# Kernel tuning notes

Hardware: AMD Instinct MI355X
Metric: run time of the kernel (lower is better)

## Reference

```python
import jax, jax.numpy as jnp
import numpy as np

N_NODES = 100_000
N_EDGES = 1_600_000
F_NODE = 4
F_EDGE = 5
H = 64
EDGE_DIM = 2 * H + F_EDGE  # 133


def setup_inputs() -> dict:
    key = jax.random.key(0)
    ks = jax.random.split(key, 24)
    s = 0.05
    inp = {
        "node_feat": jax.random.normal(ks[0], (N_NODES, F_NODE), jnp.float32),
        "edge_feat": jax.random.normal(ks[1], (N_EDGES, F_EDGE), jnp.float32),
        "src": jax.random.randint(ks[2], (N_EDGES,), 0, N_NODES, jnp.int32),
        "dst": jax.random.randint(ks[3], (N_EDGES,), 0, N_NODES, jnp.int32),
        # SAGEConv 1 (DGL mean aggregator: fc_self(h) + fc_neigh(mean_neigh(h)) + bias)
        "W1s": jax.random.normal(ks[4], (F_NODE, H), jnp.float32) * s,
        "W1n": jax.random.normal(ks[5], (F_NODE, H), jnp.float32) * s,
        "b1": jnp.zeros((H,), jnp.float32),
        # SAGEConv 2
        "W2s": jax.random.normal(ks[6], (H, H), jnp.float32) * s,
        "W2n": jax.random.normal(ks[7], (H, H), jnp.float32) * s,
        "b2": jnp.zeros((H,), jnp.float32),
        # nodeprocess: Linear(F_NODE? no -> applied to h which is H-dim) Linear(H? )
        # NOTE: original declares nn.Linear(num_node_features, hidden) but applies it to h (H-dim);
        # we follow the applied shape, Linear(H, H), so the math is runnable and consistent.
        "Wnp": jax.random.normal(ks[8], (H, H), jnp.float32) * s,
        "bnp": jnp.zeros((H,), jnp.float32),
        # edgeprocess: Linear(EDGE_DIM, H) -> tanh -> Linear(H, 1)
        "We1": jax.random.normal(ks[9], (EDGE_DIM, H), jnp.float32) * s,
        "be1": jnp.zeros((H,), jnp.float32),
        "We2": jax.random.normal(ks[10], (H, 1), jnp.float32) * s,
        "be2": jnp.zeros((1,), jnp.float32),
        # lin1: Linear(EDGE_DIM, H); lin2: Linear(H, 1)
        "Wl1": jax.random.normal(ks[11], (EDGE_DIM, H), jnp.float32) * s,
        "bl1": jnp.zeros((H,), jnp.float32),
        "Wl2": jax.random.normal(ks[12], (H, 1), jnp.float32) * s,
        "bl2": jnp.zeros((1,), jnp.float32),
    }
    return inp


def _sage_mean(h, src, dst, Ws, Wn, b, inv_deg):
    # project first (cheaper: N x d instead of E x d), then gather+scatter-mean
    msg = (h @ Wn)[src]                                    # [E, H]
    agg = jax.ops.segment_sum(msg, dst, num_segments=h.shape[0]) * inv_deg
    return h @ Ws + agg + b


def reference(node_feat, edge_feat, src, dst,
              W1s, W1n, b1, W2s, W2n, b2,
              Wnp, bnp, We1, be1, We2, be2,
              Wl1, bl1, Wl2, bl2):
    n = node_feat.shape[0]
    deg = jax.ops.segment_sum(jnp.ones_like(dst, jnp.float32), dst, num_segments=n)
    inv_deg = (1.0 / jnp.maximum(deg, 1.0))[:, None]       # [N,1]

    h = jax.nn.relu(_sage_mean(node_feat, src, dst, W1s, W1n, b1, inv_deg))
    h = jax.nn.relu(_sage_mean(h, src, dst, W2s, W2n, b2, inv_deg))

    h_src = jax.nn.relu(h[src] @ Wnp + bnp)                # [E, H]
    h_dst = jax.nn.relu(h[dst] @ Wnp + bnp)                # [E, H]
    ef = jnp.concatenate([h_src, h_dst, edge_feat], axis=1)  # [E, 133]

    w = jax.nn.sigmoid(jnp.tanh(ef @ We1 + be1) @ We2 + be2)  # [E, 1]
    efw = ef * w
    out = jax.nn.relu(efw @ Wl1 + bl1)                     # dropout: eval mode (identity)
    return out @ Wl2 + bl2                                 # [E, 1]
```

## Files before the change

### kernel.cpp

```cpp
#include <hip/hip_runtime.h>
#include <math.h>


typedef __attribute__((ext_vector_type(8))) short bf16x8;
typedef __attribute__((ext_vector_type(4))) float f32x4;

__device__ __forceinline__ float fast_tanh(float x) {
    x = fminf(fmaxf(x, -15.f), 15.f);
    float e2 = __expf(2.f * x);
    return (e2 - 1.f) * __builtin_amdgcn_rcpf(e2 + 1.f);
}
__device__ __forceinline__ float fast_sigmoid(float x) {
    x = fminf(fmaxf(x, -60.f), 60.f);
    return __builtin_amdgcn_rcpf(1.f + __expf(-x));
}
__device__ __forceinline__ unsigned short f2bf(float f) {
    unsigned u = __float_as_uint(f);
    u = u + 0x7FFFu + ((u >> 16) & 1u);
    return (unsigned short)(u >> 16);
}
__device__ __forceinline__ unsigned pack2bf(float lo, float hi) {
    return ((unsigned)f2bf(hi) << 16) | (unsigned)f2bf(lo);
}
__device__ __forceinline__ float bflo(unsigned u) { return __uint_as_float(u << 16); }
__device__ __forceinline__ float bfhi(unsigned u) { return __uint_as_float(u & 0xFFFF0000u); }
__device__ __forceinline__ float bf2f(unsigned short h) {
    return __uint_as_float((unsigned)h << 16);
}

__device__ __forceinline__ f32x4 mfma16(uint4 a, uint4 b, f32x4 c) {
    return __builtin_amdgcn_mfma_f32_16x16x32_bf16(
        __builtin_bit_cast(bf16x8, a), __builtin_bit_cast(bf16x8, b), c, 0, 0, 0);
}

__device__ __forceinline__ float dpp_sum16(float x) {
    int t;
    t = __builtin_amdgcn_update_dpp(0, __float_as_int(x), 0xB1, 0xF, 0xF, true);
    x += __int_as_float(t);
    t = __builtin_amdgcn_update_dpp(0, __float_as_int(x), 0x4E, 0xF, 0xF, true);
    x += __int_as_float(t);
    t = __builtin_amdgcn_update_dpp(0, __float_as_int(x), 0x141, 0xF, 0xF, true);
    x += __int_as_float(t);
    t = __builtin_amdgcn_update_dpp(0, __float_as_int(x), 0x140, 0xF, 0xF, true);
    x += __int_as_float(t);
    return x;
}

__global__ void rank_k(const int* __restrict__ dst, int* __restrict__ deg,
                       int* __restrict__ rank, int E) {
    int e = blockIdx.x * blockDim.x + threadIdx.x;
    if (e < E) rank[e] = atomicAdd(&deg[dst[e]], 1);
}

__global__ void scan1_k(const int* __restrict__ deg, int* __restrict__ off,
                        int* __restrict__ bsum, int N) {
    __shared__ int tmp[256];
    int i = blockIdx.x * 256 + threadIdx.x;
    int v = (i < N) ? deg[i] : 0;
    tmp[threadIdx.x] = v;
    __syncthreads();
#pragma unroll
    for (int s = 1; s < 256; s <<= 1) {
        int t = (threadIdx.x >= s) ? tmp[threadIdx.x - s] : 0;
        __syncthreads();
        tmp[threadIdx.x] += t;
        __syncthreads();
    }
    if (i < N) off[i] = tmp[threadIdx.x] - v;
    if (threadIdx.x == 255) bsum[blockIdx.x] = tmp[255];
}

__global__ void scan2_k(int* __restrict__ bsum, int nb) {
    __shared__ int tmp[512];
    int i = threadIdx.x;
    int v = (i < nb) ? bsum[i] : 0;
    tmp[i] = v;
    __syncthreads();
#pragma unroll
    for (int s = 1; s < 512; s <<= 1) {
        int t = (i >= s) ? tmp[i - s] : 0;
        __syncthreads();
        tmp[i] += t;
        __syncthreads();
    }
    if (i < nb) bsum[i] = tmp[i] - v;
}

__global__ void scan3_k(int* __restrict__ off, const int* __restrict__ bsum,
                        int N, int E) {
    int i = blockIdx.x * 256 + threadIdx.x;
    if (i < N) off[i] += bsum[blockIdx.x];
    if (i == 0) off[N] = E;
}

__global__ void fill2_k(const int* __restrict__ src, const int* __restrict__ dst,
                        const int* __restrict__ off, const int* __restrict__ rank,
                        int4* __restrict__ slot4, int E) {
    int e = blockIdx.x * blockDim.x + threadIdx.x;
    if (e >= E) return;
    int d = dst[e];
    int pos = off[d] + rank[e];
    slot4[pos] = make_int4(src[e], e, d, 0);
}

__global__ void prep_w_k(const float* __restrict__ W2s, const float* __restrict__ W2n,
                         const float* __restrict__ Wnp, const float* __restrict__ We1,
                         const float* __restrict__ Wl1, uint4* __restrict__ w2sF,
                         uint4* __restrict__ w2nF, uint4* __restrict__ wnpF,
                         uint4* __restrict__ wbigF) {
    const int b = blockIdx.x, t = threadIdx.x;
    if (b < 3) {
        const float* W = (b == 0) ? W2s : (b == 1) ? W2n : Wnp;
        uint4* out = (b == 0) ? w2sF : (b == 1) ? w2nF : wnpF;
        for (int u = t; u < 2 * 4 * 64; u += 256) {
            int l = u & 63, nt = (u >> 6) & 3, ks = u >> 8;
            int m = nt * 16 + (l & 15), kb = ks * 32 + (l >> 4) * 8;
            unsigned hi[4], lo[4];
#pragma unroll
            for (int jp = 0; jp < 4; ++jp) {
                float v0 = W[(kb + 2 * jp) * 64 + m];
                float v1 = W[(kb + 2 * jp + 1) * 64 + m];
                unsigned short h0 = f2bf(v0), h1 = f2bf(v1);
                unsigned short q0 = f2bf(v0 - bf2f(h0)), q1 = f2bf(v1 - bf2f(h1));
                hi[jp] = ((unsigned)h1 << 16) | h0;
                lo[jp] = ((unsigned)q1 << 16) | q0;
            }
            out[u * 2]     = make_uint4(hi[0], hi[1], hi[2], hi[3]);
            out[u * 2 + 1] = make_uint4(lo[0], lo[1], lo[2], lo[3]);
        }
    } else {
        for (int u = t; u < 2 * 16 * 64; u += 256) {
            int l = u & 63, nt = (u >> 6) & 15, ks = u >> 10;
            int m = nt * 16 + (l & 15), kb = ks * 32 + (l >> 4) * 8;
            int half = m >> 7, cc = m & 127, jj = cc >> 1, p = cc & 1;
            const float* W = p ? Wl1 : We1;
            unsigned hi[4], lo[4];
#pragma unroll
            for (int jp = 0; jp < 4; ++jp) {
                float v0 = W[(half * 64 + kb + 2 * jp) * 64 + jj];
                float v1 = W[(half * 64 + kb + 2 * jp + 1) * 64 + jj];
                unsigned short h0 = f2bf(v0), h1 = f2bf(v1);
                unsigned short q0 = f2bf(v0 - bf2f(h0)), q1 = f2bf(v1 - bf2f(h1));
                hi[jp] = ((unsigned)h1 << 16) | h0;
                lo[jp] = ((unsigned)q1 << 16) | q0;
            }
            wbigF[u * 2]     = make_uint4(hi[0], hi[1], hi[2], hi[3]);
            wbigF[u * 2 + 1] = make_uint4(lo[0], lo[1], lo[2], lo[3]);
        }
    }
}

__global__ __launch_bounds__(256, 8)
void aggh1f_k(const int* __restrict__ off, const int4* __restrict__ slot4,
              const float* __restrict__ nf,
              const float* __restrict__ W1s, const float* __restrict__ W1n,
              const float* __restrict__ b1, unsigned* __restrict__ h1b, int N) {
    int n = blockIdx.x * 16 + (threadIdx.x >> 4);
    if (n >= N) return;
    int q = threadIdx.x & 15;
    int s0 = off[n], s1 = off[n + 1];
    const float4* nf4 = (const float4*)nf;
    float4 a = {0.f, 0.f, 0.f, 0.f};
    int i = s0 + q;
    int nx = (i < s1) ? slot4[i].x : 0;
    for (; i < s1; ) {
        int cur = nx;
        int in = i + 16;
        if (in < s1) nx = slot4[in].x;
        float4 r = nf4[(unsigned)cur];
        a.x += r.x; a.y += r.y; a.z += r.z; a.w += r.w;
        i = in;
    }
    a.x = dpp_sum16(a.x);
    a.y = dpp_sum16(a.y);
    a.z = dpp_sum16(a.z);
    a.w = dpp_sum16(a.w);
    float invd = 1.f / fmaxf((float)(s1 - s0), 1.f);
    a.x *= invd; a.y *= invd; a.z *= invd; a.w *= invd;
    float4 r = nf4[(unsigned)n];
    const int j0 = q << 2;
    float4 acc = *(const float4*)&b1[j0];
#pragma unroll
    for (int k = 0; k < 4; ++k) {
        float rk = (k == 0) ? r.x : (k == 1) ? r.y : (k == 2) ? r.z : r.w;
        float ak = (k == 0) ? a.x : (k == 1) ? a.y : (k == 2) ? a.z : a.w;
        float4 ws = *(const float4*)&W1s[k * 64 + j0];
        float4 wn = *(const float4*)&W1n[k * 64 + j0];
        acc.x = fmaf(rk, ws.x, acc.x); acc.y = fmaf(rk, ws.y, acc.y);
        acc.z = fmaf(rk, ws.z, acc.z); acc.w = fmaf(rk, ws.w, acc.w);
        acc.x = fmaf(ak, wn.x, acc.x); acc.y = fmaf(ak, wn.y, acc.y);
        acc.z = fmaf(ak, wn.z, acc.z); acc.w = fmaf(ak, wn.w, acc.w);
    }
    uint2 pk;
    pk.x = pack2bf(fmaxf(acc.x, 0.f), fmaxf(acc.y, 0.f));
    pk.y = pack2bf(fmaxf(acc.z, 0.f), fmaxf(acc.w, 0.f));
    *(uint2*)&h1b[(unsigned)n * 32u + (q << 1)] = pk;
}

__global__ __launch_bounds__(256, 8)
void gatherh1_k(const int* __restrict__ off, const int4* __restrict__ slot4,
                const uint4* __restrict__ h1b4, uint4* __restrict__ ah1b4, int N) {
    int n = blockIdx.x * 4 + (threadIdx.x >> 6);
    if (n >= N) return;
    int l = threadIdx.x & 63;
    int g = l >> 3, q = l & 7;
    int s0 = off[n], s1 = off[n + 1];
    float a0 = 0.f, a1 = 0.f, a2 = 0.f, a3 = 0.f;
    float a4 = 0.f, a5 = 0.f, a6 = 0.f, a7 = 0.f;
    int i = s0;
    int nA = 0, nB = 0;
    if (i + 16 <= s1) { nA = slot4[i + g].x; nB = slot4[i + 8 + g].x; }
    for (; i + 16 <= s1; ) {
        int cA = nA, cB = nB;
        int in = i + 16;
        if (in + 16 <= s1) {
            nA = slot4[in + g].x;
            nB = slot4[in + 8 + g].x;
        }
        uint4 v0 = h1b4[(unsigned)cA * 8u + q];
        uint4 v1 = h1b4[(unsigned)cB * 8u + q];
        a0 += bflo(v0.x) + bflo(v1.x); a1 += bfhi(v0.x) + bfhi(v1.x);
        a2 += bflo(v0.y) + bflo(v1.y); a3 += bfhi(v0.y) + bfhi(v1.y);
        a4 += bflo(v0.z) + bflo(v1.z); a5 += bfhi(v0.z) + bfhi(v1.z);
        a6 += bflo(v0.w) + bflo(v1.w); a7 += bfhi(v0.w) + bfhi(v1.w);
        i = in;
    }
    for (; i + 8 <= s1; i += 8) {
        int r = slot4[i + g].x;
        uint4 v = h1b4[(unsigned)r * 8u + q];
        a0 += bflo(v.x); a1 += bfhi(v.x);
        a2 += bflo(v.y); a3 += bfhi(v.y);
        a4 += bflo(v.z); a5 += bfhi(v.z);
        a6 += bflo(v.w); a7 += bfhi(v.w);
    }
    int rem = s1 - i;
    if (g < rem) {
        int r = slot4[i + g].x;
        uint4 v = h1b4[(unsigned)r * 8u + q];
        a0 += bflo(v.x); a1 += bfhi(v.x);
        a2 += bflo(v.y); a3 += bfhi(v.y);
        a4 += bflo(v.z); a5 += bfhi(v.z);
        a6 += bflo(v.w); a7 += bfhi(v.w);
    }
#pragma unroll
    for (int m = 8; m <= 32; m <<= 1) {
        a0 += __shfl_xor(a0, m); a1 += __shfl_xor(a1, m);
        a2 += __shfl_xor(a2, m); a3 += __shfl_xor(a3, m);
        a4 += __shfl_xor(a4, m); a5 += __shfl_xor(a5, m);
        a6 += __shfl_xor(a6, m); a7 += __shfl_xor(a7, m);
    }
    if (l < 8) {
        float invd = 1.f / fmaxf((float)(s1 - s0), 1.f);
        uint4 pk;
        pk.x = pack2bf(a0 * invd, a1 * invd);
        pk.y = pack2bf(a2 * invd, a3 * invd);
        pk.z = pack2bf(a4 * invd, a5 * invd);
        pk.w = pack2bf(a6 * invd, a7 * invd);
        ah1b4[(unsigned)n * 8u + q] = pk;
    }
}

__global__ __launch_bounds__(256)
void node_mlp_mfma_k(const uint4* __restrict__ h1v, const uint4* __restrict__ ahv,
                     const uint4* __restrict__ w2sF, const uint4* __restrict__ w2nF,
                     const uint4* __restrict__ wnpF, const uint4* __restrict__ wbigF,
                     const float* __restrict__ b2, const float* __restrict__ bnp,
                     const float* __restrict__ be1, unsigned short* __restrict__ ST,
                     int N) {
    __shared__ __align__(16) unsigned short Ahi[64][72];
    __shared__ __align__(16) unsigned short Alo[64][72];
    const int t = threadIdx.x;
    const int w = t >> 6, l = t & 63;
    const int lr = l & 15, kq = l >> 4;
    const int m0 = blockIdx.x * 64;
    const int gr = m0 + w * 16 + lr;
    const bool inb = gr < N;
    const int prow = w * 16 + lr;
    const int cbq = kq * 4;

    const uint4 z4 = make_uint4(0u, 0u, 0u, 0u);

    uint4 x1[2], xa[2];
#pragma unroll
    for (int ks = 0; ks < 2; ++ks) {
        unsigned idx = (unsigned)gr * 8u + (unsigned)(ks * 4 + kq);
        x1[ks] = inb ? h1v[idx] : z4;
        xa[ks] = inb ? ahv[idx] : z4;
    }

    f32x4 acc[4];
#pragma unroll
    for (int nt = 0; nt < 4; ++nt) acc[nt] = (f32x4){0.f, 0.f, 0.f, 0.f};
#pragma unroll
    for (int ks = 0; ks < 2; ++ks)
#pragma unroll
        for (int nt = 0; nt < 4; ++nt) {
            int base = ((ks * 4 + nt) * 64 + l) * 2;
            acc[nt] = mfma16(w2sF[base],     x1[ks], acc[nt]);
            acc[nt] = mfma16(w2sF[base + 1], x1[ks], acc[nt]);
            acc[nt] = mfma16(w2nF[base],     xa[ks], acc[nt]);
            acc[nt] = mfma16(w2nF[base + 1], xa[ks], acc[nt]);
        }
#pragma unroll
    for (int nt = 0; nt < 4; ++nt) {
        float4 vb = *(const float4*)&b2[nt * 16 + cbq];
        float v0 = fmaxf(acc[nt][0] + vb.x, 0.f);
        float v1 = fmaxf(acc[nt][1] + vb.y, 0.f);
        float v2 = fmaxf(acc[nt][2] + vb.z, 0.f);
        float v3 = fmaxf(acc[nt][3] + vb.w, 0.f);
        unsigned short h0 = f2bf(v0), h1 = f2bf(v1), h2 = f2bf(v2), h3 = f2bf(v3);
        unsigned short q0 = f2bf(v0 - bf2f(h0)), q1 = f2bf(v1 - bf2f(h1));
        unsigned short q2 = f2bf(v2 - bf2f(h2)), q3 = f2bf(v3 - bf2f(h3));
        *(uint2*)&Ahi[prow][nt * 16 + cbq] =
            make_uint2(((unsigned)h1 << 16) | h0, ((unsigned)h3 << 16) | h2);
        *(uint2*)&Alo[prow][nt * 16 + cbq] =
            make_uint2(((unsigned)q1 << 16) | q0, ((unsigned)q3 << 16) | q2);
    }
    __syncthreads();

    uint4 ahi2[2], alo2[2];
#pragma unroll
    for (int ks = 0; ks < 2; ++ks) {
        ahi2[ks] = *(const uint4*)&Ahi[prow][ks * 32 + kq * 8];
        alo2[ks] = *(const uint4*)&Alo[prow][ks * 32 + kq * 8];
    }

    f32x4 a3[4];
#pragma unroll
    for (int nt = 0; nt < 4; ++nt) a3[nt] = (f32x4){0.f, 0.f, 0.f, 0.f};
#pragma unroll
    for (int ks = 0; ks < 2; ++ks)
#pragma unroll
        for (int nt = 0; nt < 4; ++nt) {
            int base = ((ks * 4 + nt) * 64 + l) * 2;
            a3[nt] = mfma16(wnpF[base],     ahi2[ks], a3[nt]);
            a3[nt] = mfma16(wnpF[base + 1], ahi2[ks], a3[nt]);
            a3[nt] = mfma16(wnpF[base],     alo2[ks], a3[nt]);
        }
#pragma unroll
    for (int nt = 0; nt < 4; ++nt) {
        float4 vb = *(const float4*)&bnp[nt * 16 + cbq];
        float v0 = fmaxf(a3[nt][0] + vb.x, 0.f);
        float v1 = fmaxf(a3[nt][1] + vb.y, 0.f);
        float v2 = fmaxf(a3[nt][2] + vb.z, 0.f);
        float v3 = fmaxf(a3[nt][3] + vb.w, 0.f);
        unsigned short h0 = f2bf(v0), h1 = f2bf(v1), h2 = f2bf(v2), h3 = f2bf(v3);
        unsigned short q0 = f2bf(v0 - bf2f(h0)), q1 = f2bf(v1 - bf2f(h1));
        unsigned short q2 = f2bf(v2 - bf2f(h2)), q3 = f2bf(v3 - bf2f(h3));
        *(uint2*)&Ahi[prow][nt * 16 + cbq] =
            make_uint2(((unsigned)h1 << 16) | h0, ((unsigned)h3 << 16) | h2);
        *(uint2*)&Alo[prow][nt * 16 + cbq] =
            make_uint2(((unsigned)q1 << 16) | q0, ((unsigned)q3 << 16) | q2);
    }
    __syncthreads();

    uint4 bhi[2], blo[2];
#pragma unroll
    for (int ks = 0; ks < 2; ++ks) {
        bhi[ks] = *(const uint4*)&Ahi[prow][ks * 32 + kq * 8];
        blo[ks] = *(const uint4*)&Alo[prow][ks * 32 + kq * 8];
    }

#pragma unroll
    for (int mtg = 0; mtg < 4; ++mtg) {
        f32x4 a4[4];
#pragma unroll
        for (int m4 = 0; m4 < 4; ++m4) a4[m4] = (f32x4){0.f, 0.f, 0.f, 0.f};
#pragma unroll
        for (int m4 = 0; m4 < 4; ++m4) {
            int mt = mtg * 4 + m4;
#pragma unroll
            for (int ks = 0; ks < 2; ++ks) {
                int base = ((ks * 16 + mt) * 64 + l) * 2;
                a4[m4] = mfma16(wbigF[base],     bhi[ks], a4[m4]);
                a4[m4] = mfma16(wbigF[base + 1], bhi[ks], a4[m4]);
                a4[m4] = mfma16(wbigF[base],     blo[ks], a4[m4]);
            }
        }
#pragma unroll
        for (int m4 = 0; m4 < 4; ++m4) {
            int mt = mtg * 4 + m4;
            int stcb = mt * 16 + cbq;
            float v0 = a4[m4][0], v1 = a4[m4][1], v2 = a4[m4][2], v3 = a4[m4][3];
            if (mt >= 8) {
                int jj0 = (mt - 8) * 8 + kq * 2;
                v0 += be1[jj0];
                v2 += be1[jj0 + 1];
            }
            ushort4 pk;
            pk.x = f2bf(v0); pk.y = f2bf(v1); pk.z = f2bf(v2); pk.w = f2bf(v3);
            if (inb) *(ushort4*)&ST[(unsigned)gr * 256u + (unsigned)stcb] = pk;
        }
    }
}

struct P8 {
    int2 seA, seB;
    uint4 pwA, swA, pwB, swB;
    float eA0, eA1, eA2, eA3, eA4;
    float eB0, eB1, eB2, eB3, eB4;
    bool actA, actB;
};

__device__ __forceinline__ P8 pref_pair(int c, int nwaves, int nch, int E,
                                        int g, int j0,
                                        const int4* __restrict__ slot4,
                                        const float* __restrict__ ef,
                                        const unsigned* __restrict__ ST32) {
    P8 p;
    int sA = c * 4 + g;
    int cB = c + nwaves;
    int sB = cB * 4 + g;
    p.actA = (c < nch) && (sA < E);
    p.actB = (cB < nch) && (sB < E);
    unsigned uA = p.actA ? (unsigned)sA : 0u;
    unsigned uB = p.actB ? (unsigned)sB : 0u;
    int4 svA = slot4[uA];
    int4 svB = slot4[uB];
    p.seA = make_int2(svA.x, svA.y);
    p.seB = make_int2(svB.x, svB.y);
    p.pwA = *(const uint4*)&ST32[(unsigned)svA.z * 128u + 64u + (unsigned)j0];
    p.pwB = *(const uint4*)&ST32[(unsigned)svB.z * 128u + 64u + (unsigned)j0];
    p.swA = *(const uint4*)&ST32[(unsigned)svA.x * 128u + (unsigned)j0];
    p.swB = *(const uint4*)&ST32[(unsigned)svB.x * 128u + (unsigned)j0];
    const float* epA = ef + (unsigned)svA.y * 5u;
    const float* epB = ef + (unsigned)svB.y * 5u;
    p.eA0 = epA[0]; p.eA1 = epA[1]; p.eA2 = epA[2]; p.eA3 = epA[3]; p.eA4 = epA[4];
    p.eB0 = epB[0]; p.eB1 = epB[1]; p.eB2 = epB[2]; p.eB3 = epB[3]; p.eB4 = epB[4];
    return p;
}

__global__ void edge_k(const int4* __restrict__ slot4,
                       const float* __restrict__ ef, const unsigned* __restrict__ ST32,
                       const float* __restrict__ We1,
                       const float* __restrict__ We2, const float* __restrict__ be2,
                       const float* __restrict__ Wl1, const float* __restrict__ bl1,
                       const float* __restrict__ Wl2, const float* __restrict__ bl2,
                       float* __restrict__ out, int E, int nwaves) {
    const int l = threadIdx.x & 63;
    const int g = l >> 4;
    const int q = l & 15;
    const int j0 = q << 2;
    const int wid = blockIdx.x * (blockDim.x >> 6) + (threadIdx.x >> 6);

    float4 wet[5], wlt[5];
#pragma unroll
    for (int k = 0; k < 5; ++k) {
        wet[k] = *(const float4*)&We1[(128 + k) * 64 + j0];
        wlt[k] = *(const float4*)&Wl1[(128 + k) * 64 + j0];
    }
    const float4 vwe2 = *(const float4*)&We2[j0];
    const float4 vbl1 = *(const float4*)&bl1[j0];
    const float4 vwl2 = *(const float4*)&Wl2[j0];
    const float vbe2 = be2[0], vbl2 = bl2[0];

    const int nch = (E + 3) >> 2;
    const int step = 2 * nwaves;

#define KS(EK, K) \
    t4.x = fmaf(EK, wet[K].x, t4.x); t4.y = fmaf(EK, wet[K].y, t4.y); \
    t4.z = fmaf(EK, wet[K].z, t4.z); t4.w = fmaf(EK, wet[K].w, t4.w); \
    u4.x = fmaf(EK, wlt[K].x, u4.x); u4.y = fmaf(EK, wlt[K].y, u4.y); \
    u4.z = fmaf(EK, wlt[K].z, u4.z); u4.w = fmaf(EK, wlt[K].w, u4.w);

    P8 p = pref_pair(wid, nwaves, nch, E, g, j0, slot4, ef, ST32);
    for (int c = wid; c < nch; ) {
        int cn = c + step;
        P8 pn = pref_pair(cn, nwaves, nch, E, g, j0, slot4, ef, ST32);

        {
            float4 t4 = {bflo(p.swA.x) + bflo(p.pwA.x),
                         bflo(p.swA.y) + bflo(p.pwA.y),
                         bflo(p.swA.z) + bflo(p.pwA.z),
                         bflo(p.swA.w) + bflo(p.pwA.w)};
            float4 u4 = {bfhi(p.swA.x) + bfhi(p.pwA.x), bfhi(p.swA.y) + bfhi(p.pwA.y),
                         bfhi(p.swA.z) + bfhi(p.pwA.z), bfhi(p.swA.w) + bfhi(p.pwA.w)};
            KS(p.eA0, 0) KS(p.eA1, 1) KS(p.eA2, 2) KS(p.eA3, 3) KS(p.eA4, 4)
            float z = fast_tanh(t4.x) * vwe2.x + fast_tanh(t4.y) * vwe2.y
                    + fast_tanh(t4.z) * vwe2.z + fast_tanh(t4.w) * vwe2.w;
            z = dpp_sum16(z);
            float w = fast_sigmoid(z + vbe2);
            float o = fmaxf(fmaf(w, u4.x, vbl1.x), 0.f) * vwl2.x
                    + fmaxf(fmaf(w, u4.y, vbl1.y), 0.f) * vwl2.y
                    + fmaxf(fmaf(w, u4.z, vbl1.z), 0.f) * vwl2.z
                    + fmaxf(fmaf(w, u4.w, vbl1.w), 0.f) * vwl2.w;
            o = dpp_sum16(o);
            if (q == 0 && p.actA) out[(unsigned)p.seA.y] = o + vbl2;
        }
        {
            float4 t4 = {bflo(p.swB.x) + bflo(p.pwB.x),
                         bflo(p.swB.y) + bflo(p.pwB.y),
                         bflo(p.swB.z) + bflo(p.pwB.z),
                         bflo(p.swB.w) + bflo(p.pwB.w)};
            float4 u4 = {bfhi(p.swB.x) + bfhi(p.pwB.x), bfhi(p.swB.y) + bfhi(p.pwB.y),
                         bfhi(p.swB.z) + bfhi(p.pwB.z), bfhi(p.swB.w) + bfhi(p.pwB.w)};
            KS(p.eB0, 0) KS(p.eB1, 1) KS(p.eB2, 2) KS(p.eB3, 3) KS(p.eB4, 4)
            float z = fast_tanh(t4.x) * vwe2.x + fast_tanh(t4.y) * vwe2.y
                    + fast_tanh(t4.z) * vwe2.z + fast_tanh(t4.w) * vwe2.w;
            z = dpp_sum16(z);
            float w = fast_sigmoid(z + vbe2);
            float o = fmaxf(fmaf(w, u4.x, vbl1.x), 0.f) * vwl2.x
                    + fmaxf(fmaf(w, u4.y, vbl1.y), 0.f) * vwl2.y
                    + fmaxf(fmaf(w, u4.z, vbl1.z), 0.f) * vwl2.z
                    + fmaxf(fmaf(w, u4.w, vbl1.w), 0.f) * vwl2.w;
            o = dpp_sum16(o);
            if (q == 0 && p.actB) out[(unsigned)p.seB.y] = o + vbl2;
        }
        p = pn;
        c = cn;
    }
#undef KS
}

extern "C" void kernel_launch(void* const* d_in, const int* in_sizes, int n_in,
                              void* d_out, int out_size, void* d_ws, size_t ws_size,
                              hipStream_t stream) {
    const float* nf  = (const float*)d_in[0];
    const float* ef  = (const float*)d_in[1];
    const int*   src = (const int*)d_in[2];
    const int*   dst = (const int*)d_in[3];
    const float* W1s = (const float*)d_in[4];
    const float* W1n = (const float*)d_in[5];
    const float* b1  = (const float*)d_in[6];
    const float* W2s = (const float*)d_in[7];
    const float* W2n = (const float*)d_in[8];
    const float* b2  = (const float*)d_in[9];
    const float* Wnp = (const float*)d_in[10];
    const float* bnp = (const float*)d_in[11];
    const float* We1 = (const float*)d_in[12];
    const float* be1 = (const float*)d_in[13];
    const float* We2 = (const float*)d_in[14];
    const float* be2 = (const float*)d_in[15];
    const float* Wl1 = (const float*)d_in[16];
    const float* bl1 = (const float*)d_in[17];
    const float* Wl2 = (const float*)d_in[18];
    const float* bl2 = (const float*)d_in[19];

    const int N = in_sizes[0] / 4;
    const int E = in_sizes[2];

    float* wsf = (float*)d_ws;
    unsigned short* ST = (unsigned short*)wsf;
    unsigned* ah1b = (unsigned*)(wsf + (size_t)128 * N);
    uint4* w2sF  = (uint4*)(wsf + (size_t)160 * N);
    uint4* w2nF  = w2sF + 1024;
    uint4* wnpF  = w2sF + 2048;
    uint4* wbigF = w2sF + 3072;
    unsigned* h1b  = (unsigned*)(wsf + (size_t)160 * N + 28672);
    int4* slot4 = (int4*)(wsf + (size_t)192 * N + 28672);
    int*  rank = (int*)(wsf + (size_t)256 * N + 28672);
    int*  deg  = (int*)(wsf + (size_t)272 * N + 28672);
    int*  off  = deg + N;
    int*  bsum = off + N + 1;
    float* out = (float*)d_out;

    const int nblkN1 = (N + 255) / 256;
    const int nblkE  = (E + 255) / 256;
    const int nblkNw4 = (N + 3) / 4;
    const int nblkN16 = (N + 15) / 16;
    const int gemmx  = (N + 63) / 64;
    const int EDGE_BLOCKS = 3072;
    const int nwaves = EDGE_BLOCKS * 4;

    prep_w_k<<<4, 256, 0, stream>>>(W2s, W2n, Wnp, We1, Wl1,
                                    w2sF, w2nF, wnpF, wbigF);

    hipMemsetAsync(deg, 0, (size_t)N * sizeof(int), stream);
    rank_k<<<nblkE, 256, 0, stream>>>(dst, deg, rank, E);
    scan1_k<<<nblkN1, 256, 0, stream>>>(deg, off, bsum, N);
    scan2_k<<<1, 512, 0, stream>>>(bsum, nblkN1);
    scan3_k<<<nblkN1, 256, 0, stream>>>(off, bsum, N, E);
    fill2_k<<<nblkE, 256, 0, stream>>>(src, dst, off, rank, slot4, E);

    aggh1f_k<<<nblkN16, 256, 0, stream>>>(off, slot4, nf, W1s, W1n, b1, h1b, N);

    gatherh1_k<<<nblkNw4, 256, 0, stream>>>(off, slot4, (const uint4*)h1b,
                                            (uint4*)ah1b, N);

    node_mlp_mfma_k<<<gemmx, 256, 0, stream>>>((const uint4*)h1b, (const uint4*)ah1b,
                                               w2sF, w2nF, wnpF, wbigF,
                                               b2, bnp, be1, ST, N);

    edge_k<<<EDGE_BLOCKS, 256, 0, stream>>>(slot4, ef, (const unsigned*)ST,
                                            We1, We2, be2, Wl1, bl1, Wl2, bl2,
                                            out, E, nwaves);
}
```

Measured before the change: 451.0 us.

## Compute edge-feature projection in edge kernel with MFMA instead of scalar FMAs

```diff
diff --git a/kernel.cpp b/kernel.cpp
--- a/kernel.cpp
+++ b/kernel.cpp
@@ -107,7 +107,7 @@
                          const float* __restrict__ Wnp, const float* __restrict__ We1,
                          const float* __restrict__ Wl1, uint4* __restrict__ w2sF,
                          uint4* __restrict__ w2nF, uint4* __restrict__ wnpF,
-                         uint4* __restrict__ wbigF) {
+                         uint4* __restrict__ wbigF, uint4* __restrict__ efragT) {
     const int b = blockIdx.x, t = threadIdx.x;
     if (b < 3) {
         const float* W = (b == 0) ? W2s : (b == 1) ? W2n : Wnp;
@@ -128,7 +128,7 @@
             out[u * 2]     = make_uint4(hi[0], hi[1], hi[2], hi[3]);
             out[u * 2 + 1] = make_uint4(lo[0], lo[1], lo[2], lo[3]);
         }
-    } else {
+    } else if (b == 3) {
         for (int u = t; u < 2 * 16 * 64; u += 256) {
             int l = u & 63, nt = (u >> 6) & 15, ks = u >> 10;
             int m = nt * 16 + (l & 15), kb = ks * 32 + (l >> 4) * 8;
@@ -146,6 +146,27 @@
             }
             wbigF[u * 2]     = make_uint4(hi[0], hi[1], hi[2], hi[3]);
             wbigF[u * 2 + 1] = make_uint4(lo[0], lo[1], lo[2], lo[3]);
+        }
+    } else {
+        for (int u = t; u < 8 * 64; u += 256) {
+            int l = u & 63, tile = u >> 6;
+            int kq = l >> 4, m16 = l & 15;
+            const float* W = (tile < 4) ? We1 : Wl1;
+            int c = (tile & 3) * 16 + m16;
+            unsigned uu0 = 0u, uu1 = 0u, uu2 = 0u;
+            if (kq < 2) {
+                float v[5];
+#pragma unroll
+                for (int j = 0; j < 5; ++j) {
+                    float wv = W[(128 + j) * 64 + c];
+                    unsigned short h = f2bf(wv);
+                    v[j] = (kq == 0) ? bf2f(h) : (wv - bf2f(h));
+                }
+                uu0 = pack2bf(v[0], v[1]);
+                uu1 = pack2bf(v[2], v[3]);
+                uu2 = pack2bf(v[4], 0.f);
+            }
+            efragT[tile * 64 + l] = make_uint4(uu0, uu1, uu2, 0u);
         }
     }
 }
@@ -394,122 +415,106 @@
     }
 }
 
-struct P8 {
-    int2 seA, seB;
-    uint4 pwA, swA, pwB, swB;
-    float eA0, eA1, eA2, eA3, eA4;
-    float eB0, eB1, eB2, eB3, eB4;
-    bool actA, actB;
-};
-
-__device__ __forceinline__ P8 pref_pair(int c, int nwaves, int nch, int E,
-                                        int g, int j0,
-                                        const int4* __restrict__ slot4,
-                                        const float* __restrict__ ef,
-                                        const unsigned* __restrict__ ST32) {
-    P8 p;
-    int sA = c * 4 + g;
-    int cB = c + nwaves;
-    int sB = cB * 4 + g;
-    p.actA = (c < nch) && (sA < E);
-    p.actB = (cB < nch) && (sB < E);
-    unsigned uA = p.actA ? (unsigned)sA : 0u;
-    unsigned uB = p.actB ? (unsigned)sB : 0u;
-    int4 svA = slot4[uA];
-    int4 svB = slot4[uB];
-    p.seA = make_int2(svA.x, svA.y);
-    p.seB = make_int2(svB.x, svB.y);
-    p.pwA = *(const uint4*)&ST32[(unsigned)svA.z * 128u + 64u + (unsigned)j0];
-    p.pwB = *(const uint4*)&ST32[(unsigned)svB.z * 128u + 64u + (unsigned)j0];
-    p.swA = *(const uint4*)&ST32[(unsigned)svA.x * 128u + (unsigned)j0];
-    p.swB = *(const uint4*)&ST32[(unsigned)svB.x * 128u + (unsigned)j0];
-    const float* epA = ef + (unsigned)svA.y * 5u;
-    const float* epB = ef + (unsigned)svB.y * 5u;
-    p.eA0 = epA[0]; p.eA1 = epA[1]; p.eA2 = epA[2]; p.eA3 = epA[3]; p.eA4 = epA[4];
-    p.eB0 = epB[0]; p.eB1 = epB[1]; p.eB2 = epB[2]; p.eB3 = epB[3]; p.eB4 = epB[4];
-    return p;
-}
-
-__global__ void edge_k(const int4* __restrict__ slot4,
-                       const float* __restrict__ ef, const unsigned* __restrict__ ST32,
-                       const float* __restrict__ We1,
-                       const float* __restrict__ We2, const float* __restrict__ be2,
-                       const float* __restrict__ Wl1, const float* __restrict__ bl1,
-                       const float* __restrict__ Wl2, const float* __restrict__ bl2,
-                       float* __restrict__ out, int E, int nwaves) {
+__global__ __launch_bounds__(256)
+void edge_k(const int4* __restrict__ slot4, const float* __restrict__ ef,
+            const unsigned* __restrict__ ST32, const uint4* __restrict__ efragT,
+            const float* __restrict__ We2, const float* __restrict__ be2,
+            const float* __restrict__ bl1, const float* __restrict__ Wl2,
+            const float* __restrict__ bl2, float* __restrict__ out,
+            int E, int nwaves) {
     const int l = threadIdx.x & 63;
-    const int g = l >> 4;
-    const int q = l & 15;
-    const int j0 = q << 2;
+    const int e4 = l & 15;
+    const int rg = l >> 4;
+    const int rg4 = rg << 2;
     const int wid = blockIdx.x * (blockDim.x >> 6) + (threadIdx.x >> 6);
-
-    float4 wet[5], wlt[5];
-#pragma unroll
-    for (int k = 0; k < 5; ++k) {
-        wet[k] = *(const float4*)&We1[(128 + k) * 64 + j0];
-        wlt[k] = *(const float4*)&Wl1[(128 + k) * 64 + j0];
-    }
-    const float4 vwe2 = *(const float4*)&We2[j0];
-    const float4 vbl1 = *(const float4*)&bl1[j0];
-    const float4 vwl2 = *(const float4*)&Wl2[j0];
+    const int ng = (E + 15) >> 4;
     const float vbe2 = be2[0], vbl2 = bl2[0];
-
-    const int nch = (E + 3) >> 2;
-    const int step = 2 * nwaves;
-
-#define KS(EK, K) \
-    t4.x = fmaf(EK, wet[K].x, t4.x); t4.y = fmaf(EK, wet[K].y, t4.y); \
-    t4.z = fmaf(EK, wet[K].z, t4.z); t4.w = fmaf(EK, wet[K].w, t4.w); \
-    u4.x = fmaf(EK, wlt[K].x, u4.x); u4.y = fmaf(EK, wlt[K].y, u4.y); \
-    u4.z = fmaf(EK, wlt[K].z, u4.z); u4.w = fmaf(EK, wlt[K].w, u4.w);
-
-    P8 p = pref_pair(wid, nwaves, nch, E, g, j0, slot4, ef, ST32);
-    for (int c = wid; c < nch; ) {
-        int cn = c + step;
-        P8 pn = pref_pair(cn, nwaves, nch, E, g, j0, slot4, ef, ST32);
-
+    const bool bzero = rg >= 2;
+    const uint4 z4u = make_uint4(0u, 0u, 0u, 0u);
+    const f32x4 zf = {0.f, 0.f, 0.f, 0.f};
+
+    int4 sv; uint4 bfr; bool act;
+    {
+        int s = wid * 16 + e4;
+        act = (wid < ng) && (s < E);
+        sv = slot4[act ? (unsigned)s : 0u];
+        const float* ep = ef + (unsigned)sv.y * 5u;
+        unsigned b0 = pack2bf(ep[0], ep[1]);
+        unsigned b1 = pack2bf(ep[2], ep[3]);
+        unsigned b2 = pack2bf(ep[4], 0.f);
+        bfr = bzero ? z4u : make_uint4(b0, b1, b2, 0u);
+    }
+
+    for (int g = wid; g < ng; ) {
+        int gn = g + nwaves;
+        int4 svn; uint4 bfn; bool actn;
         {
-            float4 t4 = {bflo(p.swA.x) + bflo(p.pwA.x),
-                         bflo(p.swA.y) + bflo(p.pwA.y),
-                         bflo(p.swA.z) + bflo(p.pwA.z),
-                         bflo(p.swA.w) + bflo(p.pwA.w)};
-            float4 u4 = {bfhi(p.swA.x) + bfhi(p.pwA.x), bfhi(p.swA.y) + bfhi(p.pwA.y),
-                         bfhi(p.swA.z) + bfhi(p.pwA.z), bfhi(p.swA.w) + bfhi(p.pwA.w)};
-            KS(p.eA0, 0) KS(p.eA1, 1) KS(p.eA2, 2) KS(p.eA3, 3) KS(p.eA4, 4)
-            float z = fast_tanh(t4.x) * vwe2.x + fast_tanh(t4.y) * vwe2.y
-                    + fast_tanh(t4.z) * vwe2.z + fast_tanh(t4.w) * vwe2.w;
-            z = dpp_sum16(z);
-            float w = fast_sigmoid(z + vbe2);
-            float o = fmaxf(fmaf(w, u4.x, vbl1.x), 0.f) * vwl2.x
-                    + fmaxf(fmaf(w, u4.y, vbl1.y), 0.f) * vwl2.y
-                    + fmaxf(fmaf(w, u4.z, vbl1.z), 0.f) * vwl2.z
-                    + fmaxf(fmaf(w, u4.w, vbl1.w), 0.f) * vwl2.w;
-            o = dpp_sum16(o);
-            if (q == 0 && p.actA) out[(unsigned)p.seA.y] = o + vbl2;
-        }
-        {
-            float4 t4 = {bflo(p.swB.x) + bflo(p.pwB.x),
-                         bflo(p.swB.y) + bflo(p.pwB.y),
-                         bflo(p.swB.z) + bflo(p.pwB.z),
-                         bflo(p.swB.w) + bflo(p.pwB.w)};
-            float4 u4 = {bfhi(p.swB.x) + bfhi(p.pwB.x), bfhi(p.swB.y) + bfhi(p.pwB.y),
-                         bfhi(p.swB.z) + bfhi(p.pwB.z), bfhi(p.swB.w) + bfhi(p.pwB.w)};
-            KS(p.eB0, 0) KS(p.eB1, 1) KS(p.eB2, 2) KS(p.eB3, 3) KS(p.eB4, 4)
-            float z = fast_tanh(t4.x) * vwe2.x + fast_tanh(t4.y) * vwe2.y
-                    + fast_tanh(t4.z) * vwe2.z + fast_tanh(t4.w) * vwe2.w;
-            z = dpp_sum16(z);
-            float w = fast_sigmoid(z + vbe2);
-            float o = fmaxf(fmaf(w, u4.x, vbl1.x), 0.f) * vwl2.x
-                    + fmaxf(fmaf(w, u4.y, vbl1.y), 0.f) * vwl2.y
-                    + fmaxf(fmaf(w, u4.z, vbl1.z), 0.f) * vwl2.z
-                    + fmaxf(fmaf(w, u4.w, vbl1.w), 0.f) * vwl2.w;
-            o = dpp_sum16(o);
-            if (q == 0 && p.actB) out[(unsigned)p.seB.y] = o + vbl2;
-        }
-        p = pn;
-        c = cn;
-    }
-#undef KS
+            int s = gn * 16 + e4;
+            actn = (gn < ng) && (s < E);
+            svn = slot4[actn ? (unsigned)s : 0u];
+            const float* ep = ef + (unsigned)svn.y * 5u;
+            unsigned b0 = pack2bf(ep[0], ep[1]);
+            unsigned b1 = pack2bf(ep[2], ep[3]);
+            unsigned b2 = pack2bf(ep[4], 0.f);
+            bfn = bzero ? z4u : make_uint4(b0, b1, b2, 0u);
+        }
+
+        unsigned srb = (unsigned)sv.x * 128u + (unsigned)rg4;
+        unsigned drb = (unsigned)sv.z * 128u + 64u + (unsigned)rg4;
+        uint4 sw0 = *(const uint4*)&ST32[srb];
+        uint4 sw1 = *(const uint4*)&ST32[srb + 16u];
+        uint4 sw2 = *(const uint4*)&ST32[srb + 32u];
+        uint4 sw3 = *(const uint4*)&ST32[srb + 48u];
+        uint4 pw0 = *(const uint4*)&ST32[drb];
+        uint4 pw1 = *(const uint4*)&ST32[drb + 16u];
+        uint4 pw2 = *(const uint4*)&ST32[drb + 32u];
+        uint4 pw3 = *(const uint4*)&ST32[drb + 48u];
+
+        f32x4 dt0 = mfma16(efragT[0 * 64 + l], bfr, zf);
+        f32x4 dt1 = mfma16(efragT[1 * 64 + l], bfr, zf);
+        f32x4 dt2 = mfma16(efragT[2 * 64 + l], bfr, zf);
+        f32x4 dt3 = mfma16(efragT[3 * 64 + l], bfr, zf);
+        f32x4 du0 = mfma16(efragT[4 * 64 + l], bfr, zf);
+        f32x4 du1 = mfma16(efragT[5 * 64 + l], bfr, zf);
+        f32x4 du2 = mfma16(efragT[6 * 64 + l], bfr, zf);
+        f32x4 du3 = mfma16(efragT[7 * 64 + l], bfr, zf);
+
+        float z = 0.f;
+#define TT(i, DT, SW, PW) { \
+        float4 w2v = *(const float4*)&We2[(i) * 16 + rg4]; \
+        z = fmaf(fast_tanh(DT[0] + bflo(SW.x) + bflo(PW.x)), w2v.x, z); \
+        z = fmaf(fast_tanh(DT[1] + bflo(SW.y) + bflo(PW.y)), w2v.y, z); \
+        z = fmaf(fast_tanh(DT[2] + bflo(SW.z) + bflo(PW.z)), w2v.z, z); \
+        z = fmaf(fast_tanh(DT[3] + bflo(SW.w) + bflo(PW.w)), w2v.w, z); }
+        TT(0, dt0, sw0, pw0)
+        TT(1, dt1, sw1, pw1)
+        TT(2, dt2, sw2, pw2)
+        TT(3, dt3, sw3, pw3)
+#undef TT
+        z += __shfl_xor(z, 16);
+        z += __shfl_xor(z, 32);
+        float w = fast_sigmoid(z + vbe2);
+
+        float o = 0.f;
+#define UT(i, DU, SW, PW) { \
+        float4 blv = *(const float4*)&bl1[(i) * 16 + rg4]; \
+        float4 wlv = *(const float4*)&Wl2[(i) * 16 + rg4]; \
+        o = fmaf(fmaxf(fmaf(w, DU[0] + bfhi(SW.x) + bfhi(PW.x), blv.x), 0.f), wlv.x, o); \
+        o = fmaf(fmaxf(fmaf(w, DU[1] + bfhi(SW.y) + bfhi(PW.y), blv.y), 0.f), wlv.y, o); \
+        o = fmaf(fmaxf(fmaf(w, DU[2] + bfhi(SW.z) + bfhi(PW.z), blv.z), 0.f), wlv.z, o); \
+        o = fmaf(fmaxf(fmaf(w, DU[3] + bfhi(SW.w) + bfhi(PW.w), blv.w), 0.f), wlv.w, o); }
+        UT(0, du0, sw0, pw0)
+        UT(1, du1, sw1, pw1)
+        UT(2, du2, sw2, pw2)
+        UT(3, du3, sw3, pw3)
+#undef UT
+        o += __shfl_xor(o, 16);
+        o += __shfl_xor(o, 32);
+        if (rg == 0 && act) out[(unsigned)sv.y] = o + vbl2;
+
+        sv = svn; bfr = bfn; act = actn;
+        g = gn;
+    }
 }
 
 extern "C" void kernel_launch(void* const* d_in, const int* in_sizes, int n_in,
@@ -542,14 +547,15 @@
     float* wsf = (float*)d_ws;
     unsigned short* ST = (unsigned short*)wsf;
     unsigned* ah1b = (unsigned*)(wsf + (size_t)128 * N);
-    uint4* w2sF  = (uint4*)(wsf + (size_t)160 * N);
-    uint4* w2nF  = w2sF + 1024;
-    uint4* wnpF  = w2sF + 2048;
-    uint4* wbigF = w2sF + 3072;
-    unsigned* h1b  = (unsigned*)(wsf + (size_t)160 * N + 28672);
-    int4* slot4 = (int4*)(wsf + (size_t)192 * N + 28672);
-    int*  rank = (int*)(wsf + (size_t)256 * N + 28672);
-    int*  deg  = (int*)(wsf + (size_t)272 * N + 28672);
+    uint4* w2sF   = (uint4*)(wsf + (size_t)160 * N);
+    uint4* w2nF   = w2sF + 1024;
+    uint4* wnpF   = w2sF + 2048;
+    uint4* wbigF  = w2sF + 3072;
+    uint4* efragT = w2sF + 7168;
+    unsigned* h1b  = (unsigned*)(wsf + (size_t)160 * N + 30720);
+    int4* slot4 = (int4*)(wsf + (size_t)192 * N + 30720);
+    int*  rank = (int*)(wsf + (size_t)256 * N + 30720);
+    int*  deg  = (int*)(wsf + (size_t)272 * N + 30720);
     int*  off  = deg + N;
     int*  bsum = off + N + 1;
     float* out = (float*)d_out;
@@ -562,8 +568,8 @@
     const int EDGE_BLOCKS = 3072;
     const int nwaves = EDGE_BLOCKS * 4;
 
-    prep_w_k<<<4, 256, 0, stream>>>(W2s, W2n, Wnp, We1, Wl1,
-                                    w2sF, w2nF, wnpF, wbigF);
+    prep_w_k<<<5, 256, 0, stream>>>(W2s, W2n, Wnp, We1, Wl1,
+                                    w2sF, w2nF, wnpF, wbigF, efragT);
 
     hipMemsetAsync(deg, 0, (size_t)N * sizeof(int), stream);
     rank_k<<<nblkE, 256, 0, stream>>>(dst, deg, rank, E);
@@ -582,6 +588,6 @@
                                                b2, bnp, be1, ST, N);
 
     edge_k<<<EDGE_BLOCKS, 256, 0, stream>>>(slot4, ef, (const unsigned*)ST,
-                                            We1, We2, be2, Wl1, bl1, Wl2, bl2,
+                                            efragT, We2, be2, bl1, Wl2, bl2,
                                             out, E, nwaves);
 }
```

After: 447.6 us (median of 2 runs). About the same (-0.7%).
